# Kernel optimization log

Measured on AMD Instinct MI355X. Metric: run time of the kernel, lower is better.

Reference implementation:

```python
import jax, jax.numpy as jnp
import numpy as np

K, N = 4096, 4096
GROUP_SIZE = 64
N_GROUPS = N // GROUP_SIZE
B, S = 4, 2048
NBITS = 4


def setup_inputs() -> dict:
    key = jax.random.key(0)
    ks = jax.random.split(key, 7)
    x = jax.random.normal(ks[0], (B, S, N), dtype=jnp.float32)
    # per-group scales/zeros broadcast over the group_size axis
    scales = jax.random.uniform(ks[1], (K, N_GROUPS, 1), dtype=jnp.float32, minval=0.001, maxval=0.05)
    zeros = jax.random.uniform(ks[2], (K, N_GROUPS, 1), dtype=jnp.float32, minval=0.0, maxval=2.0 ** NBITS - 1)
    mu1 = jax.random.uniform(ks[3], (N,), dtype=jnp.float32, minval=0.5, maxval=1.5)
    mu2 = jax.random.uniform(ks[4], (K,), dtype=jnp.float32, minval=0.5, maxval=1.5)
    bias = jax.random.normal(ks[5], (K,), dtype=jnp.float32)
    W_q = jax.random.randint(ks[6], (K, N), 0, 2 ** NBITS, dtype=jnp.int32)
    return {"x": x, "scales": scales, "zeros": zeros, "mu1": mu1, "mu2": mu2, "bias": bias, "W_q": W_q}


def reference(x, scales, zeros, mu1, mu2, bias, W_q):
    # dequantize: per-group (Q - zero) * scale, then Sinkhorn rescale mu2 (rows) * mu1 (cols)
    k, n = W_q.shape
    n_groups = scales.shape[1]
    Qg = W_q.astype(jnp.float32).reshape(k, n_groups, -1)  # [K, G, gs]
    W_deq = ((Qg - zeros) * scales).reshape(k, n) * mu2[:, None] * mu1[None, :]
    W_deq = W_deq.astype(x.dtype)
    # nn.functional.linear: x @ W^T + b
    return jnp.einsum('bsn,kn->bsk', x, W_deq) + bias
```

## Files before the change

kernel.cpp:

```cpp
#include <hip/hip_runtime.h>
#include <hip/hip_bf16.h>
#include <stdint.h>
#include <type_traits>

typedef unsigned short u16;
typedef __bf16 bf16x8 __attribute__((ext_vector_type(8)));
typedef float f32x4 __attribute__((ext_vector_type(4)));

#define M_TOT 8192
#define N_TOT 4096
#define K_TOT 4096
#define BM 256
#define BN 256
#define BK 64
#define NT 64

#define HALF_EL 8192
#define B_OFF   16384
#define SLOT_EL 32768
#define SLOT_BYTES 65536

#define CVT_BLOCKS 16384
#define DEQ_BLOCKS 8192

template <int V> using ic = std::integral_constant<int, V>;
template <bool V> using bc = std::integral_constant<bool, V>;

__device__ __forceinline__ u16 f2bf(float f) {
    union { float f; uint32_t u; } v; v.f = f;
    uint32_t u = v.u;
    return (u16)((u + 0x7fffu + ((u >> 16) & 1u)) >> 16);
}

__global__ __launch_bounds__(256) void prep_kernel(const float* __restrict__ x,
                                                   u16* __restrict__ xb,
                                                   const int* __restrict__ wq,
                                                   const float* __restrict__ scales,
                                                   const float* __restrict__ zeros,
                                                   const float* __restrict__ mu1,
                                                   const float* __restrict__ mu2,
                                                   u16* __restrict__ wb) {
    const int b = blockIdx.x;
    if (b < CVT_BLOCKS) {
        const int i = b * 256 + threadIdx.x;
        const float4* p = (const float4*)x + (size_t)i * 2;
        float4 v0 = p[0], v1 = p[1];
        uint4 o;
        o.x = (uint32_t)f2bf(v0.x) | ((uint32_t)f2bf(v0.y) << 16);
        o.y = (uint32_t)f2bf(v0.z) | ((uint32_t)f2bf(v0.w) << 16);
        o.z = (uint32_t)f2bf(v1.x) | ((uint32_t)f2bf(v1.y) << 16);
        o.w = (uint32_t)f2bf(v1.z) | ((uint32_t)f2bf(v1.w) << 16);
        *((uint4*)(xb + (size_t)i * 8)) = o;
    } else {
        const int i = (b - CVT_BLOCKS) * 256 + threadIdx.x;
        const int k  = i >> 9;
        const int n0 = (i & 511) << 3;
        const int g  = n0 >> 6;
        const float z  = zeros[k * 64 + g];
        const float sm = scales[k * 64 + g] * mu2[k];
        const int4* qp = (const int4*)(wq + (size_t)k * N_TOT + n0);
        int4 q0 = qp[0], q1 = qp[1];
        const float4* mp = (const float4*)(mu1 + n0);
        float4 u0 = mp[0], u1 = mp[1];
        uint4 o;
        o.x = (uint32_t)f2bf(((float)q0.x - z) * sm * u0.x) |
              ((uint32_t)f2bf(((float)q0.y - z) * sm * u0.y) << 16);
        o.y = (uint32_t)f2bf(((float)q0.z - z) * sm * u0.z) |
              ((uint32_t)f2bf(((float)q0.w - z) * sm * u0.w) << 16);
        o.z = (uint32_t)f2bf(((float)q1.x - z) * sm * u1.x) |
              ((uint32_t)f2bf(((float)q1.y - z) * sm * u1.y) << 16);
        o.w = (uint32_t)f2bf(((float)q1.z - z) * sm * u1.z) |
              ((uint32_t)f2bf(((float)q1.w - z) * sm * u1.w) << 16);
        *((uint4*)(wb + (size_t)k * N_TOT + n0)) = o;
    }
}

__global__ __launch_bounds__(512, 2) void gemm_kernel(const u16* __restrict__ Xb,
                                                      const u16* __restrict__ Wb,
                                                      const float* __restrict__ bias,
                                                      float* __restrict__ out) {
    __shared__ __align__(16) u16 lds[2 * SLOT_EL];

    const int bid = blockIdx.x;
    const int cpx = gridDim.x >> 3;
    const int swz = (bid & 7) * cpx + (bid >> 3);
    const int bm = swz >> 4;
    const int bn = swz & 15;

    const int tid  = threadIdx.x;
    const int w    = tid >> 6;
    const int lane = tid & 63;
    const int wm = w >> 2, wn = w & 3;

    const int scol = (((lane & 7) ^ (lane >> 3)) << 3);
    const u16* aT = Xb + (size_t)(bm * BM + w * 16 + (lane >> 3)) * N_TOT + scol;
    const u16* bT = Wb + (size_t)(bn * BN + w * 16 + (lane >> 3)) * N_TOT + scol;

    u16* const sdA = &lds[w * 1024];
    u16* const sdB = &lds[B_OFF + w * 1024];

    auto gload = [](const u16* s, u16* d) {
        __builtin_amdgcn_global_load_lds(
            (const __attribute__((address_space(1))) uint32_t*)s,
            (__attribute__((address_space(3))) uint32_t*)d, 16, 0, 0);
    };
    auto stA = [&](auto SlC, auto Hc, auto Dc) {
        const u16* s = aT + (size_t)(Hc.value * 128) * N_TOT + Dc.value;
        u16* d = sdA + SlC.value * SLOT_EL + Hc.value * HALF_EL;
        gload(s, d); gload(s + (size_t)8 * N_TOT, d + 512);
    };
    auto stB = [&](auto SlC, auto Hc, auto Dc) {
        const u16* s = bT + (size_t)(Hc.value * 128) * N_TOT + Dc.value;
        u16* d = sdB + SlC.value * SLOT_EL + Hc.value * HALF_EL;
        gload(s, d); gload(s + (size_t)8 * N_TOT, d + 512);
    };

    const int cc0 = (((lane >> 4) << 3)) ^ ((lane & 7) << 3);
    const int rA  = ((wm << 4) + (lane & 15)) << 6;
    const int rB  = ((wn << 4) + (lane & 15)) << 6;
    int oAa = (rA + cc0) * 2;
    int oAb = (rA + (cc0 ^ 32)) * 2;
    int oBa = (B_OFF + rB + cc0) * 2;
    int oBb = (B_OFF + rB + (cc0 ^ 32)) * 2;
    const char* const ldsc = (const char*)lds;

    f32x4 acc[2][2][4][2] = {};
    bf16x8 afLo[4][2], afHi[4][2];
    bf16x8 bf0[2][2], bf1[2][2];

    auto rd_afLo_next = [&]() {
        const int xa = oAa ^ SLOT_BYTES, xb2 = oAb ^ SLOT_BYTES;
        #pragma unroll
        for (int j = 0; j < 4; ++j) {
            afLo[j][0] = *(const bf16x8*)(ldsc + xa + j * 4096);
            afLo[j][1] = *(const bf16x8*)(ldsc + xb2 + j * 4096);
        }
    };
    auto rd_bf0_next = [&]() {
        const int xa = oBa ^ SLOT_BYTES, xb2 = oBb ^ SLOT_BYTES;
        #pragma unroll
        for (int j2 = 0; j2 < 2; ++j2) {
            bf0[j2][0] = *(const bf16x8*)(ldsc + xa + j2 * 8192);
            bf0[j2][1] = *(const bf16x8*)(ldsc + xb2 + j2 * 8192);
        }
    };
    auto rd_afHi_cur = [&]() {
        #pragma unroll
        for (int j = 0; j < 4; ++j) {
            afHi[j][0] = *(const bf16x8*)(ldsc + oAa + 16384 + j * 4096);
            afHi[j][1] = *(const bf16x8*)(ldsc + oAb + 16384 + j * 4096);
        }
    };
    auto rd_bf1_cur = [&]() {
        #pragma unroll
        for (int j2 = 0; j2 < 2; ++j2) {
            bf1[j2][0] = *(const bf16x8*)(ldsc + oBa + 16384 + j2 * 8192);
            bf1[j2][1] = *(const bf16x8*)(ldsc + oBb + 16384 + j2 * 8192);
        }
    };

    #define MFMA_CLUSTER(A, B, MH, NH)                                          \
        __builtin_amdgcn_s_setprio(1);                                          \
        _Pragma("unroll")                                                       \
        for (int ks = 0; ks < 2; ++ks)                                          \
            _Pragma("unroll")                                                   \
            for (int j = 0; j < 4; ++j)                                         \
                _Pragma("unroll")                                               \
                for (int j2 = 0; j2 < 2; ++j2)                                  \
                    acc[MH][NH][j][j2] = __builtin_amdgcn_mfma_f32_16x16x32_bf16(\
                        A[j][ks], B[j2][ks], acc[MH][NH][j][j2], 0, 0, 0);      \
        __builtin_amdgcn_s_setprio(0);

    auto ktile = [&](auto SlC, auto Stg, auto RdN, auto V1c, auto V3c, auto Dc) {
        constexpr int SL = SlC.value;
        rd_bf1_cur();
        MFMA_CLUSTER(afLo, bf0, 0, 0)
        rd_afHi_cur();
        if constexpr (Stg.value) { stA(SlC, ic<0>{}, Dc);
                                   stB(SlC, ic<0>{}, Dc); }
        MFMA_CLUSTER(afLo, bf1, 0, 1)
        if constexpr (V1c.value == 8) asm volatile("s_waitcnt vmcnt(8)" ::: "memory");
        else if constexpr (V1c.value == 4) asm volatile("s_waitcnt vmcnt(4)" ::: "memory");
        __builtin_amdgcn_s_barrier();
        __builtin_amdgcn_sched_barrier(0);
        if constexpr (RdN.value) rd_afLo_next();
        MFMA_CLUSTER(afHi, bf1, 1, 1)
        MFMA_CLUSTER(afHi, bf0, 1, 0)
        if constexpr (RdN.value) rd_bf0_next();
        if constexpr (Stg.value) { stA(SlC, ic<1>{}, Dc);
                                   stB(SlC, ic<1>{}, Dc); }
        if constexpr (V3c.value == 8) asm volatile("s_waitcnt vmcnt(8)" ::: "memory");
        else if constexpr (V3c.value == 0) asm volatile("s_waitcnt vmcnt(0)" ::: "memory");
        __builtin_amdgcn_s_barrier();
        __builtin_amdgcn_sched_barrier(0);
        oAa ^= SLOT_BYTES; oAb ^= SLOT_BYTES; oBa ^= SLOT_BYTES; oBb ^= SLOT_BYTES;
    };

    stA(ic<0>{}, ic<0>{}, ic<0>{});  stB(ic<0>{}, ic<0>{}, ic<0>{});
    stA(ic<0>{}, ic<1>{}, ic<0>{});  stB(ic<0>{}, ic<1>{}, ic<0>{});
    stA(ic<1>{}, ic<0>{}, ic<BK>{}); stB(ic<1>{}, ic<0>{}, ic<BK>{});
    stA(ic<1>{}, ic<1>{}, ic<BK>{}); stB(ic<1>{}, ic<1>{}, ic<BK>{});
    asm volatile("s_waitcnt vmcnt(8)" ::: "memory");
    __builtin_amdgcn_s_barrier();
    __builtin_amdgcn_sched_barrier(0);
    {
        #pragma unroll
        for (int j = 0; j < 4; ++j) {
            afLo[j][0] = *(const bf16x8*)(ldsc + oAa + j * 4096);
            afLo[j][1] = *(const bf16x8*)(ldsc + oAb + j * 4096);
        }
        #pragma unroll
        for (int j2 = 0; j2 < 2; ++j2) {
            bf0[j2][0] = *(const bf16x8*)(ldsc + oBa + j2 * 8192);
            bf0[j2][1] = *(const bf16x8*)(ldsc + oBb + j2 * 8192);
        }
    }

    for (int it = 0; it < 31; ++it) {
        ktile(ic<0>{}, bc<true>{}, bc<true>{}, ic<8>{}, ic<8>{}, ic<2 * BK>{});
        ktile(ic<1>{}, bc<true>{}, bc<true>{}, ic<8>{}, ic<8>{}, ic<3 * BK>{});
        aT += 2 * BK;
        bT += 2 * BK;
    }
    ktile(ic<0>{}, bc<false>{}, bc<true>{}, ic<4>{}, ic<0>{}, ic<0>{});
    ktile(ic<1>{}, bc<false>{}, bc<false>{}, ic<-1>{}, ic<-1>{}, ic<0>{});

    #undef MFMA_CLUSTER

    #pragma unroll
    for (int mh_ = 0; mh_ < 2; ++mh_)
        #pragma unroll
        for (int j = 0; j < 4; ++j)
            #pragma unroll
            for (int rr = 0; rr < 4; ++rr) {
                const int row = bm * BM + mh_ * 128 + j * 32 + wm * 16 + ((lane >> 4) << 2) + rr;
                float* orow = out + (size_t)row * K_TOT;
                #pragma unroll
                for (int nh_ = 0; nh_ < 2; ++nh_)
                    #pragma unroll
                    for (int j2 = 0; j2 < 2; ++j2) {
                        const int col = bn * BN + nh_ * 128 + j2 * 64 + wn * 16 + (lane & 15);
                        orow[col] = acc[mh_][nh_][j][j2][rr] + bias[col];
                    }
            }
}

extern "C" void kernel_launch(void* const* d_in, const int* in_sizes, int n_in,
                              void* d_out, int out_size, void* d_ws, size_t ws_size,
                              hipStream_t stream) {
    const float* x      = (const float*)d_in[0];
    const float* scales = (const float*)d_in[1];
    const float* zeros  = (const float*)d_in[2];
    const float* mu1    = (const float*)d_in[3];
    const float* mu2    = (const float*)d_in[4];
    const float* bias   = (const float*)d_in[5];
    const int*   wq     = (const int*)d_in[6];
    float* out = (float*)d_out;

    u16* xb = (u16*)d_ws;
    u16* wb = (u16*)d_ws + (size_t)M_TOT * N_TOT;

    prep_kernel<<<CVT_BLOCKS + DEQ_BLOCKS, 256, 0, stream>>>(
        x, xb, wq, scales, zeros, mu1, mu2, wb);
    gemm_kernel<<<(M_TOT / BM) * (K_TOT / BN), 512, 0, stream>>>(xb, wb, bias, out);
}
```

Before: 264.0 us.

## Process two M tiles per GEMM block, overlapping next tile's prefetch with epilogue

Each GEMM workgroup now computes two consecutive BM row tiles for the same BN column, halving the grid from 512 to 256 blocks. The global-to-LDS prefetch of the second tile is issued before the first tile's epilogue stores, so output writes overlap with the loads for the next tile. With 256 CUs and 2 blocks per CU, this removes the partial second wave but leaves half the occupancy slots idle. Accumulators are zeroed between tiles.

Result: slower. 272.5 us (+3.2%).

```diff
diff --git a/kernel.cpp b/kernel.cpp
--- a/kernel.cpp
+++ b/kernel.cpp
@@ -84,8 +84,9 @@
     const int bid = blockIdx.x;
     const int cpx = gridDim.x >> 3;
     const int swz = (bid & 7) * cpx + (bid >> 3);
-    const int bm = swz >> 4;
-    const int bn = swz & 15;
+    const int bn  = swz & 15;
+    const int bm0 = (swz >> 4) << 1;
+    const int bm1 = bm0 + 1;
 
     const int tid  = threadIdx.x;
     const int w    = tid >> 6;
@@ -93,8 +94,8 @@
     const int wm = w >> 2, wn = w & 3;
 
     const int scol = (((lane & 7) ^ (lane >> 3)) << 3);
-    const u16* aT = Xb + (size_t)(bm * BM + w * 16 + (lane >> 3)) * N_TOT + scol;
-    const u16* bT = Wb + (size_t)(bn * BN + w * 16 + (lane >> 3)) * N_TOT + scol;
+    const u16* aT;
+    const u16* bT;
 
     u16* const sdA = &lds[w * 1024];
     u16* const sdB = &lds[B_OFF + w * 1024];
@@ -196,53 +197,89 @@
         oAa ^= SLOT_BYTES; oAb ^= SLOT_BYTES; oBa ^= SLOT_BYTES; oBb ^= SLOT_BYTES;
     };
 
-    stA(ic<0>{}, ic<0>{}, ic<0>{});  stB(ic<0>{}, ic<0>{}, ic<0>{});
-    stA(ic<0>{}, ic<1>{}, ic<0>{});  stB(ic<0>{}, ic<1>{}, ic<0>{});
-    stA(ic<1>{}, ic<0>{}, ic<BK>{}); stB(ic<1>{}, ic<0>{}, ic<BK>{});
-    stA(ic<1>{}, ic<1>{}, ic<BK>{}); stB(ic<1>{}, ic<1>{}, ic<BK>{});
+    auto stage01 = [&]() {
+        stA(ic<0>{}, ic<0>{}, ic<0>{});  stB(ic<0>{}, ic<0>{}, ic<0>{});
+        stA(ic<0>{}, ic<1>{}, ic<0>{});  stB(ic<0>{}, ic<1>{}, ic<0>{});
+        stA(ic<1>{}, ic<0>{}, ic<BK>{}); stB(ic<1>{}, ic<0>{}, ic<BK>{});
+        stA(ic<1>{}, ic<1>{}, ic<BK>{}); stB(ic<1>{}, ic<1>{}, ic<BK>{});
+    };
+    auto read_q0 = [&]() {
+        #pragma unroll
+        for (int j = 0; j < 4; ++j) {
+            afLo[j][0] = *(const bf16x8*)(ldsc + oAa + j * 4096);
+            afLo[j][1] = *(const bf16x8*)(ldsc + oAb + j * 4096);
+        }
+        #pragma unroll
+        for (int j2 = 0; j2 < 2; ++j2) {
+            bf0[j2][0] = *(const bf16x8*)(ldsc + oBa + j2 * 8192);
+            bf0[j2][1] = *(const bf16x8*)(ldsc + oBb + j2 * 8192);
+        }
+    };
+    auto kloop = [&]() {
+        for (int it = 0; it < 31; ++it) {
+            ktile(ic<0>{}, bc<true>{}, bc<true>{}, ic<8>{}, ic<8>{}, ic<2 * BK>{});
+            ktile(ic<1>{}, bc<true>{}, bc<true>{}, ic<8>{}, ic<8>{}, ic<3 * BK>{});
+            aT += 2 * BK;
+            bT += 2 * BK;
+        }
+        ktile(ic<0>{}, bc<false>{}, bc<true>{}, ic<4>{}, ic<0>{}, ic<0>{});
+        ktile(ic<1>{}, bc<false>{}, bc<false>{}, ic<-1>{}, ic<-1>{}, ic<0>{});
+    };
+    auto epilogue = [&](int bmv) {
+        #pragma unroll
+        for (int mh_ = 0; mh_ < 2; ++mh_)
+            #pragma unroll
+            for (int j = 0; j < 4; ++j)
+                #pragma unroll
+                for (int rr = 0; rr < 4; ++rr) {
+                    const int row = bmv * BM + mh_ * 128 + j * 32 + wm * 16
+                                  + ((lane >> 4) << 2) + rr;
+                    float* orow = out + (size_t)row * K_TOT;
+                    #pragma unroll
+                    for (int nh_ = 0; nh_ < 2; ++nh_)
+                        #pragma unroll
+                        for (int j2 = 0; j2 < 2; ++j2) {
+                            const int col = bn * BN + nh_ * 128 + j2 * 64
+                                          + wn * 16 + (lane & 15);
+                            orow[col] = acc[mh_][nh_][j][j2][rr] + bias[col];
+                        }
+                }
+    };
+
+    aT = Xb + (size_t)(bm0 * BM + w * 16 + (lane >> 3)) * N_TOT + scol;
+    bT = Wb + (size_t)(bn  * BN + w * 16 + (lane >> 3)) * N_TOT + scol;
+    stage01();
     asm volatile("s_waitcnt vmcnt(8)" ::: "memory");
     __builtin_amdgcn_s_barrier();
     __builtin_amdgcn_sched_barrier(0);
+    read_q0();
+    kloop();
+
+    aT = Xb + (size_t)(bm1 * BM + w * 16 + (lane >> 3)) * N_TOT + scol;
+    bT = Wb + (size_t)(bn  * BN + w * 16 + (lane >> 3)) * N_TOT + scol;
+    stage01();
+    epilogue(bm0);
     {
-        #pragma unroll
-        for (int j = 0; j < 4; ++j) {
-            afLo[j][0] = *(const bf16x8*)(ldsc + oAa + j * 4096);
-            afLo[j][1] = *(const bf16x8*)(ldsc + oAb + j * 4096);
-        }
-        #pragma unroll
-        for (int j2 = 0; j2 < 2; ++j2) {
-            bf0[j2][0] = *(const bf16x8*)(ldsc + oBa + j2 * 8192);
-            bf0[j2][1] = *(const bf16x8*)(ldsc + oBb + j2 * 8192);
-        }
+        const f32x4 zf = {};
+        #pragma unroll
+        for (int mh_ = 0; mh_ < 2; ++mh_)
+            #pragma unroll
+            for (int nh_ = 0; nh_ < 2; ++nh_)
+                #pragma unroll
+                for (int j = 0; j < 4; ++j)
+                    #pragma unroll
+                    for (int j2 = 0; j2 < 2; ++j2)
+                        acc[mh_][nh_][j][j2] = zf;
     }
-
-    for (int it = 0; it < 31; ++it) {
-        ktile(ic<0>{}, bc<true>{}, bc<true>{}, ic<8>{}, ic<8>{}, ic<2 * BK>{});
-        ktile(ic<1>{}, bc<true>{}, bc<true>{}, ic<8>{}, ic<8>{}, ic<3 * BK>{});
-        aT += 2 * BK;
-        bT += 2 * BK;
-    }
-    ktile(ic<0>{}, bc<false>{}, bc<true>{}, ic<4>{}, ic<0>{}, ic<0>{});
-    ktile(ic<1>{}, bc<false>{}, bc<false>{}, ic<-1>{}, ic<-1>{}, ic<0>{});
+    asm volatile("s_waitcnt vmcnt(0)" ::: "memory");
+    __builtin_amdgcn_s_barrier();
+    __builtin_amdgcn_sched_barrier(0);
+    read_q0();
+
+    kloop();
+    epilogue(bm1);
 
     #undef MFMA_CLUSTER
-
-    #pragma unroll
-    for (int mh_ = 0; mh_ < 2; ++mh_)
-        #pragma unroll
-        for (int j = 0; j < 4; ++j)
-            #pragma unroll
-            for (int rr = 0; rr < 4; ++rr) {
-                const int row = bm * BM + mh_ * 128 + j * 32 + wm * 16 + ((lane >> 4) << 2) + rr;
-                float* orow = out + (size_t)row * K_TOT;
-                #pragma unroll
-                for (int nh_ = 0; nh_ < 2; ++nh_)
-                    #pragma unroll
-                    for (int j2 = 0; j2 < 2; ++j2) {
-                        const int col = bn * BN + nh_ * 128 + j2 * 64 + wn * 16 + (lane & 15);
-                        orow[col] = acc[mh_][nh_][j][j2][rr] + bias[col];
-                    }
-            }
 }
 
 extern "C" void kernel_launch(void* const* d_in, const int* in_sizes, int n_in,
@@ -262,5 +299,5 @@
 
     prep_kernel<<<CVT_BLOCKS + DEQ_BLOCKS, 256, 0, stream>>>(
         x, xb, wq, scales, zeros, mu1, mu2, wb);
-    gemm_kernel<<<(M_TOT / BM) * (K_TOT / BN), 512, 0, stream>>>(xb, wb, bias, out);
+    gemm_kernel<<<(M_TOT / BM / 2) * (K_TOT / BN), 512, 0, stream>>>(xb, wb, bias, out);
 }
```
